# Optimization experiments

Measured on AMD Instinct MI355X. Metric: run time of the kernel, lower is better.

The kernel has to match this reference:

```python
import jax, jax.numpy as jnp
import numpy as np

ANCHORS = [[[116, 90], [156, 198], [373, 326]], [[30, 61], [62, 45], [59, 119]], [[10, 13], [16, 30], [33, 23]]]
INPUT_SIZE = 416.0
B, G, C = 32, 20, 80


def _decode_scale(inp, anch):
    # inp: [B, 3*(5+C), W, W]
    Bq, _, W, _ = inp.shape
    sf = INPUT_SIZE / W
    p = inp.reshape(Bq, 3, -1, W, W).transpose(0, 1, 3, 4, 2)  # [B,3,W,W,5+C]
    sx = jax.nn.sigmoid(p[..., 0])
    sy = jax.nn.sigmoid(p[..., 1])
    w = p[..., 2]
    h = p[..., 3]
    conf = jax.nn.sigmoid(p[..., 4])
    cls = jax.nn.sigmoid(p[..., 5:])
    gx = jnp.arange(W, dtype=inp.dtype)[None, None, None, :]  # varies along cols
    gy = jnp.arange(W, dtype=inp.dtype)[None, None, :, None]  # varies along rows
    a = jnp.floor(jnp.asarray(anch, dtype=inp.dtype) / sf)  # // scale_factor as in source
    aw = a[:, 0][None, :, None, None]
    ah = a[:, 1][None, :, None, None]
    bx = (sx + gx) * sf
    by = (sy + gy) * sf
    bw = jnp.exp(w) * aw * sf
    bh = jnp.exp(h) * ah * sf
    out = jnp.concatenate([bx[..., None], by[..., None], bw[..., None], bh[..., None], conf[..., None], cls], axis=-1)
    return out.reshape(Bq, -1, 5 + cls.shape[-1])  # [B, 3*W*W, 5+C]


def _forward(x0, x1, x2, batch_y):
    xs = [x0, x1, x2]
    Bq = x0.shape[0]
    img_dim = x0.shape[1] // 3
    w1 = x0.shape[-1]  # source uses width1 for ALL scales (faithful bug reproduction)
    raw = jnp.concatenate(
        [xi.reshape(Bq, 3, -1, w1, w1).transpose(0, 1, 3, 4, 2).reshape(Bq, -1, img_dim) for xi in xs], axis=1)
    dec = jnp.concatenate([_decode_scale(xi, ANCHORS[i]) for i, xi in enumerate(xs)], axis=1)  # [B,N,5+C]
    # pairwise IoU between every decoded box [B,1,N] and every GT [B,G,1]
    pb = dec[..., :4]
    px, py, pw, ph = pb[..., 0][:, None, :], pb[..., 1][:, None, :], pb[..., 2][:, None, :], pb[..., 3][:, None, :]
    gb = batch_y[..., :4]
    gxc, gyc, gw, gh = gb[..., 0][..., None], gb[..., 1][..., None], gb[..., 2][..., None], gb[..., 3][..., None]
    xl = jnp.maximum(px, gxc)
    yt = jnp.maximum(py, gyc)
    xr = jnp.minimum(px + pw, gxc + gw)
    yb = jnp.minimum(py + ph, gyc + gh)
    inter = jnp.clip(xr - xl, 0) * jnp.clip(yb - yt, 0)
    iou = inter / (pw * ph + gw * gh - inter)  # [B,G,N]
    pos = jnp.argmax(iou, axis=-1)  # [B,G] (first max, like torch.max)
    neg_mask = (iou < 0.5).astype(dec.dtype)  # [B,G,N]
    x_pos = jnp.take_along_axis(raw[..., :4], pos[..., None], axis=1)  # [B,G,4]
    conf = dec[..., 4]  # [B,N]
    conf_pos = jnp.take_along_axis(conf, pos, axis=1)  # [B,G]
    cls_pos = jnp.take_along_axis(dec[..., 5:], pos[..., None], axis=1)  # [B,G,C]
    labels = batch_y[..., 4].astype(jnp.int32)  # [B,G]
    mse = jnp.mean((x_pos - gb) ** 2, axis=-1)  # MSELoss on the single matched row
    obj = jnp.log(conf_pos + 1e-9)
    log1m = jnp.log(1.0 - conf + 1e-9)[:, None, :]  # [B,1,N]
    cnt = jnp.maximum(jnp.sum(neg_mask, axis=-1), 1.0)
    noobj = jnp.sum(neg_mask * log1m, axis=-1) / cnt  # masked mean over negatives
    ce = -jnp.take_along_axis(jax.nn.log_softmax(cls_pos, axis=-1), labels[..., None], axis=-1)[..., 0]
    # loss += box*MSE - obj*mean(log conf) - noobj*mean(log(1-conf)) - class*CE  (rates all 1)
    return jnp.sum(1.0 * mse - 1.0 * obj - 1.0 * noobj - 1.0 * ce)


def setup_inputs() -> dict:
    key = jax.random.key(0)
    k0, k1, k2, k3, k4, k5 = jax.random.split(key, 6)
    ch = 3 * (5 + C)
    x0 = jax.random.normal(k0, (B, ch, 13, 13), dtype=jnp.float32)
    x1 = jax.random.normal(k1, (B, ch, 26, 26), dtype=jnp.float32)
    x2 = jax.random.normal(k2, (B, ch, 52, 52), dtype=jnp.float32)
    xy = jax.random.uniform(k3, (B, G, 2), dtype=jnp.float32) * 350.0
    wh = jax.random.uniform(k4, (B, G, 2), dtype=jnp.float32) * 90.0 + 10.0
    lab = jax.random.randint(k5, (B, G, 1), 0, C).astype(jnp.float32)
    batch_y = jnp.concatenate([xy, wh, lab], axis=-1)  # [B,G,5]: x,y,w,h,class
    return {"x0": x0, "x1": x1, "x2": x2, "batch_y": batch_y}


def reference(x0, x1, x2, batch_y):
    return _forward(x0, x1, x2, batch_y)
```

## Files before the change

### kernel.cpp

```cpp
#include <hip/hip_runtime.h>


constexpr int B_ = 32;
constexpr int G_ = 20;
constexpr int C_ = 80;
constexpr int N_ = 10647;
constexpr int PPT = 8;
constexpr int CHUNK = 256 * PPT;
constexpr int NCHUNK = (N_ + CHUNK - 1) / CHUNK;

constexpr size_t OFF_KEY = 0;
constexpr size_t OFF_PS  = OFF_KEY + (size_t)B_ * G_ * 8;
constexpr size_t OFF_PC  = OFF_PS  + (size_t)B_ * G_ * 4;
constexpr size_t OFF_TOT = OFF_PC  + (size_t)B_ * G_ * 4;
constexpr size_t WS_NEEDED = OFF_TOT + B_ * 4;

__device__ __forceinline__ float sigm(float x) { return 1.0f / (1.0f + expf(-x)); }

__global__ __launch_bounds__(256) void init_kernel(
    unsigned long long* __restrict__ key, float* __restrict__ ps,
    float* __restrict__ pc, float* __restrict__ tot, float* __restrict__ out)
{
    const int t = threadIdx.x;
    for (int i = t; i < B_ * G_; i += 256) { key[i] = 0ull; ps[i] = 0.0f; pc[i] = 0.0f; }
    if (t < B_) tot[t] = 0.0f;
    if (t == 0) out[0] = 0.0f;
}

template <int W, int NBASE>
__device__ __forceinline__ void decode_scale(
    const float* __restrict__ x, int b, int n, float sf,
    float aw0, float aw1, float aw2, float ah0, float ah1, float ah2,
    float& x1o, float& y1o, float& x2o, float& y2o, float& area, float& l1m)
{
    constexpr int WW = W * W;
    int local = n - NBASE;
    int a   = local / WW;
    int rem = local - a * WW;
    int y   = rem / W;
    int xi  = rem - y * W;
    const float* base = x + (size_t)(b * 255 + a * 85) * WW + rem;
    float p0 = base[0];
    float p1 = base[WW];
    float p2 = base[2 * WW];
    float p3 = base[3 * WW];
    float p4 = base[4 * WW];
    float aw = (a == 0) ? aw0 : ((a == 1) ? aw1 : aw2);
    float ah = (a == 0) ? ah0 : ((a == 1) ? ah1 : ah2);
    float px = (sigm(p0) + (float)xi) * sf;
    float py = (sigm(p1) + (float)y) * sf;
    float pw = expf(p2) * aw;
    float ph = expf(p3) * ah;
    float conf = sigm(p4);
    x1o = px; y1o = py; x2o = px + pw; y2o = py + ph;
    area = pw * ph;
    l1m = logf(1.0f - conf + 1e-9f);
}

__global__ __launch_bounds__(256) void fused_kernel(
    const float* __restrict__ x0, const float* __restrict__ x1,
    const float* __restrict__ x2, const float* __restrict__ by,
    unsigned long long* __restrict__ key, float* __restrict__ ps,
    float* __restrict__ pc, float* __restrict__ tot)
{
    const int b    = blockIdx.y;
    const int base = blockIdx.x * CHUNK;
    const int tid  = threadIdx.x;

    __shared__ float s_gt[G_][5];
    __shared__ unsigned long long s_key[G_][4];
    __shared__ float s_ps[G_][4], s_pc[G_][4], s_l1m[4];

    if (tid < G_) {
        const float* yr = by + (size_t)(b * G_ + tid) * 5;
        float gxc = yr[0], gyc = yr[1], gw = yr[2], gh = yr[3];
        s_gt[tid][0] = gxc; s_gt[tid][1] = gyc;
        s_gt[tid][2] = gxc + gw; s_gt[tid][3] = gyc + gh;
        s_gt[tid][4] = gw * gh;
    }
    __syncthreads();

    float bx1[PPT], by1[PPT], bx2[PPT], by2[PPT], bar[PPT], bl1[PPT];
    float lsum = 0.0f;
    #pragma unroll
    for (int k = 0; k < PPT; ++k) {
        int n = base + k * 256 + tid;
        float X1 = 0, Y1 = 0, X2 = 0, Y2 = 0, AR = 0, L1 = 0;
        if (n < N_) {
            if (n < 507)
                decode_scale<13, 0>(x0, b, n, 32.0f, 96.0f, 128.0f, 352.0f,
                                    64.0f, 192.0f, 320.0f, X1, Y1, X2, Y2, AR, L1);
            else if (n < 2535)
                decode_scale<26, 507>(x1, b, n, 16.0f, 16.0f, 48.0f, 48.0f,
                                      48.0f, 32.0f, 112.0f, X1, Y1, X2, Y2, AR, L1);
            else
                decode_scale<52, 2535>(x2, b, n, 8.0f, 8.0f, 16.0f, 32.0f,
                                       8.0f, 24.0f, 16.0f, X1, Y1, X2, Y2, AR, L1);
        }
        bx1[k] = X1; by1[k] = Y1; bx2[k] = X2; by2[k] = Y2; bar[k] = AR; bl1[k] = L1;
        lsum += L1;
    }

    const int wave = tid >> 6;
    const int lane = tid & 63;
    for (int g = 0; g < G_; ++g) {
        float gxc = s_gt[g][0], gyc = s_gt[g][1];
        float gx2 = s_gt[g][2], gy2 = s_gt[g][3], garea = s_gt[g][4];
        float bi = -1.0f; int bidx = 0x7FFFFFFF;
        float lps = 0.0f, lpc = 0.0f;
        #pragma unroll
        for (int k = 0; k < PPT; ++k) {
            float xl = fmaxf(bx1[k], gxc);
            float yt = fmaxf(by1[k], gyc);
            float xr = fminf(bx2[k], gx2);
            float yb = fminf(by2[k], gy2);
            float inter = fmaxf(xr - xl, 0.0f) * fmaxf(yb - yt, 0.0f);
            float u = bar[k] + garea - inter;
            float iou = inter / u;
            int n = base + k * 256 + tid;
            iou = (n < N_) ? iou : -1.0f;
            if (iou > bi) { bi = iou; bidx = n; }
            if (iou >= 0.5f) { lps += bl1[k]; lpc += 1.0f; }
        }
        unsigned long long kk = (bi < 0.0f) ? 0ull
            : (((unsigned long long)__float_as_uint(bi) << 32)
               | (unsigned)(0x7FFFFFFF - bidx));
        for (int off = 32; off > 0; off >>= 1) {
            unsigned long long ok = __shfl_down(kk, off);
            float ops = __shfl_down(lps, off);
            float opc = __shfl_down(lpc, off);
            kk = (ok > kk) ? ok : kk;
            lps += ops; lpc += opc;
        }
        if (lane == 0) { s_key[g][wave] = kk; s_ps[g][wave] = lps; s_pc[g][wave] = lpc; }
    }

    for (int off = 32; off > 0; off >>= 1) lsum += __shfl_down(lsum, off);
    if (lane == 0) s_l1m[wave] = lsum;
    __syncthreads();

    if (tid < G_) {
        unsigned long long kk = s_key[tid][0];
        float lps = s_ps[tid][0], lpc = s_pc[tid][0];
        #pragma unroll
        for (int w = 1; w < 4; ++w) {
            unsigned long long ok = s_key[tid][w];
            kk = (ok > kk) ? ok : kk;
            lps += s_ps[tid][w]; lpc += s_pc[tid][w];
        }
        const int idx = b * G_ + tid;
        atomicMax(&key[idx], kk);
        atomicAdd(&ps[idx], lps);
        atomicAdd(&pc[idx], lpc);
    }
    if (tid == 0)
        atomicAdd(&tot[b], s_l1m[0] + s_l1m[1] + s_l1m[2] + s_l1m[3]);
}

__global__ __launch_bounds__(64) void epilogue_kernel(
    const float* __restrict__ x0, const float* __restrict__ x1,
    const float* __restrict__ x2, const float* __restrict__ by,
    const unsigned long long* __restrict__ key, const float* __restrict__ ps,
    const float* __restrict__ pc, const float* __restrict__ tot,
    float* __restrict__ out)
{
    const int g = blockIdx.x;
    const int b = blockIdx.y;
    const int lane = threadIdx.x;

    const unsigned long long kk = key[b * G_ + g];
    const int pos = 0x7FFFFFFF - (int)(kk & 0xFFFFFFFFull);

    const float* yrow = by + (size_t)(b * G_ + g) * 5;
    const float gxc = yrow[0], gyc = yrow[1], gw = yrow[2], gh = yrow[3];
    const int label = (int)yrow[4];

    const float* xp;
    int local, WWv;
    if (pos < 507)        { xp = x0; local = pos;        WWv = 169;  }
    else if (pos < 2535)  { xp = x1; local = pos - 507;  WWv = 676;  }
    else                  { xp = x2; local = pos - 2535; WWv = 2704; }
    const int a   = local / WWv;
    const int rem = local - a * WWv;
    const float* basep = xp + (size_t)(b * 255 + a * 85) * WWv + rem;

    float s0v = sigm(basep[(5 + lane) * WWv]);
    float s1v = -1e30f;
    if (lane < C_ - 64) s1v = sigm(basep[(5 + 64 + lane) * WWv]);
    float m = fmaxf(s0v, s1v);
    for (int off = 32; off > 0; off >>= 1) m = fmaxf(m, __shfl_xor(m, off));
    float e = expf(s0v - m) + ((lane < C_ - 64) ? expf(s1v - m) : 0.0f);
    for (int off = 32; off > 0; off >>= 1) e += __shfl_xor(e, off);

    if (lane == 0) {
        float vl = sigm(basep[(5 + label) * WWv]);
        float ce = -(vl - m - logf(e));

        float r0 = basep[0];
        float r1 = basep[WWv];
        float r2 = basep[2 * WWv];
        float r3 = basep[3 * WWv];
        float d0 = r0 - gxc, d1 = r1 - gyc, d2 = r2 - gw, d3 = r3 - gh;
        float mse = 0.25f * (d0 * d0 + d1 * d1 + d2 * d2 + d3 * d3);

        float confp = sigm(basep[4 * WWv]);
        float obj = logf(confp + 1e-9f);

        float neg_sum = tot[b] - ps[b * G_ + g];
        float neg_cnt = (float)N_ - pc[b * G_ + g];
        float noobj = neg_sum / fmaxf(neg_cnt, 1.0f);

        atomicAdd(out, mse - obj - noobj - ce);
    }
}

extern "C" void kernel_launch(void* const* d_in, const int* in_sizes, int n_in,
                              void* d_out, int out_size, void* d_ws, size_t ws_size,
                              hipStream_t stream) {
    const float* x0 = (const float*)d_in[0];
    const float* x1 = (const float*)d_in[1];
    const float* x2 = (const float*)d_in[2];
    const float* by = (const float*)d_in[3];
    float* out = (float*)d_out;

    unsigned long long* key = (unsigned long long*)((char*)d_ws + OFF_KEY);
    float* ps  = (float*)((char*)d_ws + OFF_PS);
    float* pc  = (float*)((char*)d_ws + OFF_PC);
    float* tot = (float*)((char*)d_ws + OFF_TOT);

    hipLaunchKernelGGL(init_kernel, dim3(1), dim3(256), 0, stream,
                       key, ps, pc, tot, out);
    hipLaunchKernelGGL(fused_kernel, dim3(NCHUNK, B_), dim3(256), 0, stream,
                       x0, x1, x2, by, key, ps, pc, tot);
    hipLaunchKernelGGL(epilogue_kernel, dim3(G_, B_), dim3(64), 0, stream,
                       x0, x1, x2, by, key, ps, pc, tot, out);
}
```

Baseline: 168.9 us.

## Replace global atomics with per-chunk partials, drop init kernel, use fast math intrinsics

The fused kernel now writes per-chunk partial argmax keys and sums into separate slots instead of issuing global atomics. The epilogue reduces the NCHUNK partials with wave shuffles, which makes the separate init kernel unnecessary; the output is zeroed by one thread of the fused kernel. exp, log, division and sigmoid are also swapped for hardware exp2/log/rcp intrinsics. This cuts one launch and atomic contention, at the cost of lower-precision transcendentals and slightly looser IoU tie handling.

```diff
diff --git a/kernel.cpp b/kernel.cpp
--- a/kernel.cpp
+++ b/kernel.cpp
@@ -10,22 +10,18 @@
 constexpr int NCHUNK = (N_ + CHUNK - 1) / CHUNK;
 
 constexpr size_t OFF_KEY = 0;
-constexpr size_t OFF_PS  = OFF_KEY + (size_t)B_ * G_ * 8;
-constexpr size_t OFF_PC  = OFF_PS  + (size_t)B_ * G_ * 4;
-constexpr size_t OFF_TOT = OFF_PC  + (size_t)B_ * G_ * 4;
-constexpr size_t WS_NEEDED = OFF_TOT + B_ * 4;
-
-__device__ __forceinline__ float sigm(float x) { return 1.0f / (1.0f + expf(-x)); }
-
-__global__ __launch_bounds__(256) void init_kernel(
-    unsigned long long* __restrict__ key, float* __restrict__ ps,
-    float* __restrict__ pc, float* __restrict__ tot, float* __restrict__ out)
-{
-    const int t = threadIdx.x;
-    for (int i = t; i < B_ * G_; i += 256) { key[i] = 0ull; ps[i] = 0.0f; pc[i] = 0.0f; }
-    if (t < B_) tot[t] = 0.0f;
-    if (t == 0) out[0] = 0.0f;
-}
+constexpr size_t OFF_PS  = OFF_KEY + (size_t)B_ * G_ * NCHUNK * 8;
+constexpr size_t OFF_PC  = OFF_PS  + (size_t)B_ * G_ * NCHUNK * 4;
+constexpr size_t OFF_TOT = OFF_PC  + (size_t)B_ * G_ * NCHUNK * 4;
+
+__device__ __forceinline__ float fexp(float x) {
+    return __builtin_amdgcn_exp2f(x * 1.44269504f);
+}
+__device__ __forceinline__ float flog(float x) {
+    return __builtin_amdgcn_logf(x) * 0.69314718f;
+}
+__device__ __forceinline__ float frcp(float x) { return __builtin_amdgcn_rcpf(x); }
+__device__ __forceinline__ float sigm(float x) { return frcp(1.0f + fexp(-x)); }
 
 template <int W, int NBASE>
 __device__ __forceinline__ void decode_scale(
@@ -49,23 +45,26 @@
     float ah = (a == 0) ? ah0 : ((a == 1) ? ah1 : ah2);
     float px = (sigm(p0) + (float)xi) * sf;
     float py = (sigm(p1) + (float)y) * sf;
-    float pw = expf(p2) * aw;
-    float ph = expf(p3) * ah;
+    float pw = fexp(p2) * aw;
+    float ph = fexp(p3) * ah;
     float conf = sigm(p4);
     x1o = px; y1o = py; x2o = px + pw; y2o = py + ph;
     area = pw * ph;
-    l1m = logf(1.0f - conf + 1e-9f);
+    l1m = flog(1.0f - conf + 1e-9f);
 }
 
 __global__ __launch_bounds__(256) void fused_kernel(
     const float* __restrict__ x0, const float* __restrict__ x1,
     const float* __restrict__ x2, const float* __restrict__ by,
     unsigned long long* __restrict__ key, float* __restrict__ ps,
-    float* __restrict__ pc, float* __restrict__ tot)
+    float* __restrict__ pc, float* __restrict__ tot, float* __restrict__ out)
 {
-    const int b    = blockIdx.y;
-    const int base = blockIdx.x * CHUNK;
-    const int tid  = threadIdx.x;
+    const int b     = blockIdx.y;
+    const int chunk = blockIdx.x;
+    const int base  = chunk * CHUNK;
+    const int tid   = threadIdx.x;
+
+    if (chunk == 0 && b == 0 && tid == 0) out[0] = 0.0f;
 
     __shared__ float s_gt[G_][5];
     __shared__ unsigned long long s_key[G_][4];
@@ -116,7 +115,7 @@
             float yb = fminf(by2[k], gy2);
             float inter = fmaxf(xr - xl, 0.0f) * fmaxf(yb - yt, 0.0f);
             float u = bar[k] + garea - inter;
-            float iou = inter / u;
+            float iou = inter * frcp(u);
             int n = base + k * 256 + tid;
             iou = (n < N_) ? iou : -1.0f;
             if (iou > bi) { bi = iou; bidx = n; }
@@ -148,13 +147,13 @@
             kk = (ok > kk) ? ok : kk;
             lps += s_ps[tid][w]; lpc += s_pc[tid][w];
         }
-        const int idx = b * G_ + tid;
-        atomicMax(&key[idx], kk);
-        atomicAdd(&ps[idx], lps);
-        atomicAdd(&pc[idx], lpc);
+        const int slot = (b * G_ + tid) * NCHUNK + chunk;
+        key[slot] = kk;
+        ps[slot]  = lps;
+        pc[slot]  = lpc;
     }
     if (tid == 0)
-        atomicAdd(&tot[b], s_l1m[0] + s_l1m[1] + s_l1m[2] + s_l1m[3]);
+        tot[b * NCHUNK + chunk] = s_l1m[0] + s_l1m[1] + s_l1m[2] + s_l1m[3];
 }
 
 __global__ __launch_bounds__(64) void epilogue_kernel(
@@ -168,7 +167,24 @@
     const int b = blockIdx.y;
     const int lane = threadIdx.x;
 
-    const unsigned long long kk = key[b * G_ + g];
+    unsigned long long kk = 0ull;
+    float lps = 0.0f, lpc = 0.0f, ltot = 0.0f;
+    if (lane < NCHUNK) {
+        const int slot = (b * G_ + g) * NCHUNK + lane;
+        kk  = key[slot];
+        lps = ps[slot];
+        lpc = pc[slot];
+        ltot = tot[b * NCHUNK + lane];
+    }
+    for (int off = 4; off > 0; off >>= 1) {
+        unsigned long long ok = __shfl_down(kk, off);
+        float ops = __shfl_down(lps, off);
+        float opc = __shfl_down(lpc, off);
+        float oto = __shfl_down(ltot, off);
+        kk = (ok > kk) ? ok : kk;
+        lps += ops; lpc += opc; ltot += oto;
+    }
+    kk   = __shfl(kk, 0);
     const int pos = 0x7FFFFFFF - (int)(kk & 0xFFFFFFFFull);
 
     const float* yrow = by + (size_t)(b * G_ + g) * 5;
@@ -189,12 +205,12 @@
     if (lane < C_ - 64) s1v = sigm(basep[(5 + 64 + lane) * WWv]);
     float m = fmaxf(s0v, s1v);
     for (int off = 32; off > 0; off >>= 1) m = fmaxf(m, __shfl_xor(m, off));
-    float e = expf(s0v - m) + ((lane < C_ - 64) ? expf(s1v - m) : 0.0f);
+    float e = fexp(s0v - m) + ((lane < C_ - 64) ? fexp(s1v - m) : 0.0f);
     for (int off = 32; off > 0; off >>= 1) e += __shfl_xor(e, off);
 
     if (lane == 0) {
         float vl = sigm(basep[(5 + label) * WWv]);
-        float ce = -(vl - m - logf(e));
+        float ce = -(vl - m - flog(e));
 
         float r0 = basep[0];
         float r1 = basep[WWv];
@@ -204,11 +220,11 @@
         float mse = 0.25f * (d0 * d0 + d1 * d1 + d2 * d2 + d3 * d3);
 
         float confp = sigm(basep[4 * WWv]);
-        float obj = logf(confp + 1e-9f);
-
-        float neg_sum = tot[b] - ps[b * G_ + g];
-        float neg_cnt = (float)N_ - pc[b * G_ + g];
-        float noobj = neg_sum / fmaxf(neg_cnt, 1.0f);
+        float obj = flog(confp + 1e-9f);
+
+        float neg_sum = ltot - lps;
+        float neg_cnt = (float)N_ - lpc;
+        float noobj = neg_sum * frcp(fmaxf(neg_cnt, 1.0f));
 
         atomicAdd(out, mse - obj - noobj - ce);
     }
@@ -228,10 +244,8 @@
     float* pc  = (float*)((char*)d_ws + OFF_PC);
     float* tot = (float*)((char*)d_ws + OFF_TOT);
 
-    hipLaunchKernelGGL(init_kernel, dim3(1), dim3(256), 0, stream,
-                       key, ps, pc, tot, out);
     hipLaunchKernelGGL(fused_kernel, dim3(NCHUNK, B_), dim3(256), 0, stream,
-                       x0, x1, x2, by, key, ps, pc, tot);
+                       x0, x1, x2, by, key, ps, pc, tot, out);
     hipLaunchKernelGGL(epilogue_kernel, dim3(G_, B_), dim3(64), 0, stream,
                        x0, x1, x2, by, key, ps, pc, tot, out);
 }
```

Measured after the change: 162.1 us. 4.0% less time.
